# Performance work log

Measured on AMD Instinct MI355X. Metric: run time of the kernel, lower is better.

## Reference

```python
import jax, jax.numpy as jnp
import numpy as np

B, C, HGT, WID = 4096, 64, 8, 8
NUM_HEADS, HEAD_DIM = 8, 8
LN_EPS = 1e-5


def _make_chess_bias(size=8):
    idx = np.arange(size * size)
    r, c = idx // size, idx % size
    dr = np.abs(r[:, None] - r[None, :])
    dc = np.abs(c[:, None] - c[None, :])
    dist = dr + dc
    diag = dr == dc
    bias = np.where(dist == 0, 0.1, np.where(dist <= 2, 0.05, np.where(diag, 0.03, 0.0)))
    return jnp.asarray(bias, dtype=jnp.float32)


def setup_inputs() -> dict:
    key = jax.random.key(0)
    k = jax.random.split(key, 4)
    E = C
    return {
        "x": jax.random.normal(k[0], (B, C, HGT, WID), dtype=jnp.float32),
        "pos_embed": jax.random.normal(k[1], (1, C, HGT, WID), dtype=jnp.float32),
        "ln_gamma": jnp.ones((E,), dtype=jnp.float32),
        "ln_beta": jnp.zeros((E,), dtype=jnp.float32),
        "qkv_w": jax.random.normal(k[2], (3 * E, E), dtype=jnp.float32) / np.sqrt(E),
        "qkv_b": jnp.zeros((3 * E,), dtype=jnp.float32),
        "out_w": jax.random.normal(k[3], (E, E), dtype=jnp.float32) / np.sqrt(E),
        "out_b": jnp.zeros((E,), dtype=jnp.float32),
        "chess_bias": _make_chess_bias(8),
        "stage": 1,
    }


def reference(x, pos_embed, ln_gamma, ln_beta, qkv_w, qkv_b, out_w, out_b, chess_bias, stage):
    # stage is fixed (=1); params above are the stage-1 params.
    x = x + pos_embed                                   # [B, C, H, W]
    b, c, h, w = x.shape
    x_flat = x.reshape(b, c, h * w).transpose(0, 2, 1)  # [B, S, E], S = H*W
    # LayerNorm over embed dim
    mu = jnp.mean(x_flat, axis=-1, keepdims=True)
    var = jnp.var(x_flat, axis=-1, keepdims=True)
    x_norm = (x_flat - mu) * jax.lax.rsqrt(var + LN_EPS) * ln_gamma + ln_beta
    # QKV projection (torch Linear: y = x W^T + b)
    qkv = x_norm @ qkv_w.T + qkv_b                      # [B, S, 3E]
    s = h * w
    qkv = qkv.reshape(b, s, 3, NUM_HEADS, HEAD_DIM)
    q = qkv[:, :, 0].transpose(0, 2, 1, 3)              # [B, H, S, D]
    k = qkv[:, :, 1].transpose(0, 2, 1, 3)
    v = qkv[:, :, 2].transpose(0, 2, 1, 3)
    scores = jnp.einsum("bhsd,bhtd->bhst", q, k) * (HEAD_DIM ** -0.5)
    scores = scores + chess_bias[None, None, :, :]
    attn = jax.nn.softmax(scores, axis=-1)              # dropout = identity (eval)
    out = jnp.einsum("bhst,bhtd->bhsd", attn, v)        # [B, H, S, D]
    out = out.transpose(0, 2, 1, 3).reshape(b, s, c)    # [B, S, E]
    attn_out = out @ out_w.T + out_b
    x_out = x_flat + attn_out                           # residual
    return x_out.transpose(0, 2, 1).reshape(b, c, h, w)
```

## Files before the change

### kernel.cpp

```cpp
#include <hip/hip_runtime.h>
#include <stdint.h>


typedef __attribute__((ext_vector_type(8))) __bf16 bfrag;
typedef __attribute__((ext_vector_type(4))) __bf16 bf4;
typedef __attribute__((ext_vector_type(4))) float f32x4;
typedef __attribute__((ext_vector_type(4))) uint32_t u32x4;

#define MFMA16(a, b, c) __builtin_amdgcn_mfma_f32_16x16x32_bf16((a), (b), (c), 0, 0, 0)

static __device__ __forceinline__ bfrag bsplat(float v) {
  bfrag z;
#pragma unroll
  for (int i = 0; i < 8; i++) z[i] = (__bf16)v;
  return z;
}

static __device__ __forceinline__ bfrag cvt8(const float* __restrict__ p) {
  float4 a = *(const float4*)p, b = *(const float4*)(p + 4);
  bfrag r;
  r[0] = (__bf16)a.x; r[1] = (__bf16)a.y; r[2] = (__bf16)a.z; r[3] = (__bf16)a.w;
  r[4] = (__bf16)b.x; r[5] = (__bf16)b.y; r[6] = (__bf16)b.z; r[7] = (__bf16)b.w;
  return r;
}

static __device__ __forceinline__ uint32_t pack2(float a, float b) {
  unsigned short ua = __builtin_bit_cast(unsigned short, (__bf16)a);
  unsigned short ub = __builtin_bit_cast(unsigned short, (__bf16)b);
  return (uint32_t)ua | ((uint32_t)ub << 16);
}

__global__ __launch_bounds__(256, 3) void chess_attn_kernel(
    const float* __restrict__ xg,    const float* __restrict__ posg,
    const float* __restrict__ gam,   const float* __restrict__ bet,
    const float* __restrict__ qkvw,  const float* __restrict__ qkvb,
    const float* __restrict__ outw,  const float* __restrict__ outb,
    const float* __restrict__ biasg, float* __restrict__ outg) {
  __shared__ __attribute__((aligned(16))) __bf16 P1[2][64 * 136];
  __shared__ __attribute__((aligned(16))) __bf16 P2[2][64 * 72];

  const int tid = threadIdx.x, lane = tid & 63, w = tid >> 6;
  const int m = lane & 15, g = lane >> 4;
  const int b0 = blockIdx.x * 2;
  const float LN2I = 1.4426950408889634f;
  const float SCL2 = 0.35355339059327373f * LN2I;

  {
    const float4* pp = (const float4*)(posg + (size_t)lane * 64 + w * 16);
    float4 pv[4] = {pp[0], pp[1], pp[2], pp[3]};
#pragma unroll
    for (int it = 0; it < 2; it++) {
      float* XP = (float*)P1[it];
      const float4* px = (const float4*)(xg + ((size_t)(b0 + it) * 64 + lane) * 64 + w * 16);
#pragma unroll
      for (int v = 0; v < 4; v++) {
        float4 xv = px[v];
        const int s = w * 16 + v * 4;
        XP[(s + 0) * 68 + lane] = xv.x + pv[v].x;
        XP[(s + 1) * 68 + lane] = xv.y + pv[v].y;
        XP[(s + 2) * 68 + lane] = xv.z + pv[v].z;
        XP[(s + 3) * 68 + lane] = xv.w + pv[v].w;
      }
    }
  }

  {
    const int s = tid >> 2, q = tid & 3;
    const float4* pg = (const float4*)(gam + q * 16);
    const float4* pb = (const float4*)(bet + q * 16);
    float4 g0 = pg[0], g1 = pg[1], g2 = pg[2], g3 = pg[3];
    float4 b0v = pb[0], b1 = pb[1], b2 = pb[2], b3 = pb[3];
    float gr[16] = {g0.x, g0.y, g0.z, g0.w, g1.x, g1.y, g1.z, g1.w,
                    g2.x, g2.y, g2.z, g2.w, g3.x, g3.y, g3.z, g3.w};
    float br[16] = {b0v.x, b0v.y, b0v.z, b0v.w, b1.x, b1.y, b1.z, b1.w,
                    b2.x, b2.y, b2.z, b2.w, b3.x, b3.y, b3.z, b3.w};
#pragma unroll
    for (int it = 0; it < 2; it++) {
      const float* XP = (const float*)P1[it];
      const float4* pr = (const float4*)&XP[s * 68 + q * 16];
      float4 x0 = pr[0], x1 = pr[1], x2 = pr[2], x3 = pr[3];
      float xr[16] = {x0.x, x0.y, x0.z, x0.w, x1.x, x1.y, x1.z, x1.w,
                      x2.x, x2.y, x2.z, x2.w, x3.x, x3.y, x3.z, x3.w};
      float sum = 0.f, ss = 0.f;
#pragma unroll
      for (int i = 0; i < 16; i++) { sum += xr[i]; ss = fmaf(xr[i], xr[i], ss); }
      sum += __shfl_xor(sum, 1); ss += __shfl_xor(ss, 1);
      sum += __shfl_xor(sum, 2); ss += __shfl_xor(ss, 2);
      const float mu = sum * 0.015625f;
      const float rs = __builtin_amdgcn_rsqf(ss * 0.015625f - mu * mu + 1e-5f);
      bfrag o0, o1;
#pragma unroll
      for (int i = 0; i < 8; i++) o0[i] = (__bf16)((xr[i] - mu) * rs * gr[i] + br[i]);
#pragma unroll
      for (int i = 0; i < 8; i++) o1[i] = (__bf16)((xr[8 + i] - mu) * rs * gr[8 + i] + br[8 + i]);
      *(bfrag*)&P2[it][s * 72 + q * 16] = o0;
      *(bfrag*)&P2[it][s * 72 + q * 16 + 8] = o1;
    }
  }
  __syncthreads();

  bfrag XF[2][4][2];
#pragma unroll
  for (int it = 0; it < 2; it++)
#pragma unroll
    for (int st = 0; st < 4; st++) {
      XF[it][st][0] = *(const bfrag*)&P2[it][(st * 16 + m) * 72 + g * 8];
      XF[it][st][1] = *(const bfrag*)&P2[it][(st * 16 + m) * 72 + 32 + g * 8];
    }
  __syncthreads();

  {
#pragma unroll
    for (int i = 0; i < 2; i++) {
      const int nt = w + 4 * i;
      bfrag AW0 = cvt8(qkvw + (size_t)(nt * 16 + m) * 64 + g * 8);
      bfrag AW1 = cvt8(qkvw + (size_t)(nt * 16 + m) * 64 + 32 + g * 8);
      float4 qb4 = *(const float4*)(qkvb + nt * 16 + g * 4);
#pragma unroll
      for (int it = 0; it < 2; it++)
#pragma unroll
        for (int st = 0; st < 4; st++) {
          f32x4 c = {0.f, 0.f, 0.f, 0.f};
          c = MFMA16(AW0, XF[it][st][0], c);
          c = MFMA16(AW1, XF[it][st][1], c);
          bf4 pk;
          pk[0] = (__bf16)(c[0] + qb4.x); pk[1] = (__bf16)(c[1] + qb4.y);
          pk[2] = (__bf16)(c[2] + qb4.z); pk[3] = (__bf16)(c[3] + qb4.w);
          *(bf4*)&P1[it][(st * 16 + m) * 136 + nt * 16 + g * 4] = pk;
        }
    }
    {
      const int n = 128 + w * 16 + m;
      bfrag BV0 = cvt8(qkvw + (size_t)n * 64 + g * 8);
      bfrag BV1 = cvt8(qkvw + (size_t)n * 64 + 32 + g * 8);
      const float vb = qkvb[n];
#pragma unroll
      for (int it = 0; it < 2; it++)
#pragma unroll
        for (int st = 0; st < 4; st++) {
          f32x4 c = {0.f, 0.f, 0.f, 0.f};
          c = MFMA16(XF[it][st][0], BV0, c);
          c = MFMA16(XF[it][st][1], BV1, c);
          bf4 pk;
#pragma unroll
          for (int r = 0; r < 4; r++) pk[r] = (__bf16)(c[r] + vb);
          *(bf4*)&P2[it][(w * 16 + m) * 72 + st * 16 + g * 4] = pk;
        }
    }
  }
  __syncthreads();

  const bfrag ZF  = bsplat(0.f);
  const bfrag ONE = bsplat(1.f);
  const int srcA = m + 32 * (g & 1);
  const int srcB = srcA + 16;
  const bool hi = (g >= 2);
#pragma unroll 1
  for (int hl = 0; hl < 2; hl++) {
    const int h = w + hl * 4;
    bfrag KA[2][4], VA[2][2];
#pragma unroll
    for (int it = 0; it < 2; it++) {
#pragma unroll
      for (int tt = 0; tt < 4; tt++)
        KA[it][tt] = (lane < 16) ? *(const bfrag*)&P1[it][(tt * 16 + m) * 136 + 64 + h * 8] : ZF;
#pragma unroll
      for (int kf = 0; kf < 2; kf++)
        VA[it][kf] = (m < 8) ? *(const bfrag*)&P2[it][(h * 8 + m) * 72 + kf * 32 + g * 8]
                             : ((m == 8) ? ONE : ZF);
    }
#pragma unroll
    for (int st = 0; st < 4; st++) {
      float4 bv[4];
#pragma unroll
      for (int tt = 0; tt < 4; tt++)
        bv[tt] = *(const float4*)(biasg + (size_t)(st * 16 + m) * 64 + tt * 16 + g * 4);
#pragma unroll
      for (int it = 0; it < 2; it++) {
        bfrag QB = (lane < 16) ? *(const bfrag*)&P1[it][(st * 16 + m) * 136 + h * 8] : ZF;
        f32x4 sc[4];
#pragma unroll
        for (int tt = 0; tt < 4; tt++) {
          f32x4 z = {0.f, 0.f, 0.f, 0.f};
          sc[tt] = MFMA16(KA[it][tt], QB, z);
        }
        uint32_t pk[4][2];
#pragma unroll
        for (int tt = 0; tt < 4; tt++) {
          float e0 = __builtin_amdgcn_exp2f(fmaf(bv[tt].x, LN2I, sc[tt][0] * SCL2));
          float e1 = __builtin_amdgcn_exp2f(fmaf(bv[tt].y, LN2I, sc[tt][1] * SCL2));
          float e2 = __builtin_amdgcn_exp2f(fmaf(bv[tt].z, LN2I, sc[tt][2] * SCL2));
          float e3 = __builtin_amdgcn_exp2f(fmaf(bv[tt].w, LN2I, sc[tt][3] * SCL2));
          pk[tt][0] = pack2(e0, e1);
          pk[tt][1] = pack2(e2, e3);
        }
        u32x4 U0, U1;
        {
          uint32_t a0 = __shfl((int)pk[0][0], srcA), a1 = __shfl((int)pk[1][0], srcA);
          uint32_t c0 = __shfl((int)pk[0][1], srcA), c1 = __shfl((int)pk[1][1], srcA);
          uint32_t a2 = __shfl((int)pk[0][0], srcB), a3 = __shfl((int)pk[1][0], srcB);
          uint32_t c2 = __shfl((int)pk[0][1], srcB), c3 = __shfl((int)pk[1][1], srcB);
          U0[0] = hi ? a1 : a0; U0[1] = hi ? c1 : c0;
          U0[2] = hi ? a3 : a2; U0[3] = hi ? c3 : c2;
        }
        {
          uint32_t a0 = __shfl((int)pk[2][0], srcA), a1 = __shfl((int)pk[3][0], srcA);
          uint32_t c0 = __shfl((int)pk[2][1], srcA), c1 = __shfl((int)pk[3][1], srcA);
          uint32_t a2 = __shfl((int)pk[2][0], srcB), a3 = __shfl((int)pk[3][0], srcB);
          uint32_t c2 = __shfl((int)pk[2][1], srcB), c3 = __shfl((int)pk[3][1], srcB);
          U1[0] = hi ? a1 : a0; U1[1] = hi ? c1 : c0;
          U1[2] = hi ? a3 : a2; U1[3] = hi ? c3 : c2;
        }
        bfrag PB0 = __builtin_bit_cast(bfrag, U0);
        bfrag PB1 = __builtin_bit_cast(bfrag, U1);
        f32x4 oo = {0.f, 0.f, 0.f, 0.f};
        oo = MFMA16(VA[it][0], PB0, oo);
        oo = MFMA16(VA[it][1], PB1, oo);
        const float rsum = __builtin_amdgcn_rcpf(__shfl(oo[0], 32 + m));
        bf4 ov;
#pragma unroll
        for (int r = 0; r < 4; r++) ov[r] = (__bf16)(oo[r] * rsum);
        if (g < 2) *(bf4*)&P1[it][(st * 16 + m) * 136 + 64 + h * 8 + g * 4] = ov;
      }
    }
  }
  __syncthreads();

  {
    bfrag A0[2], A1[2];
#pragma unroll
    for (int it = 0; it < 2; it++) {
      A0[it] = *(const bfrag*)&P1[it][(w * 16 + m) * 136 + 64 + g * 8];
      A1[it] = *(const bfrag*)&P1[it][(w * 16 + m) * 136 + 96 + g * 8];
    }
    const int sbase = w * 16 + g * 4;
#pragma unroll
    for (int et = 0; et < 4; et++) {
      const int e = et * 16 + m;
      bfrag BW0 = cvt8(outw + (size_t)e * 64 + g * 8);
      bfrag BW1 = cvt8(outw + (size_t)e * 64 + 32 + g * 8);
      const float ob = outb[e];
      float4 pv = *(const float4*)(posg + (size_t)e * 64 + sbase);
#pragma unroll
      for (int it = 0; it < 2; it++) {
        const size_t xoff = (size_t)(b0 + it) * 4096;
        f32x4 c = {0.f, 0.f, 0.f, 0.f};
        c = MFMA16(A0[it], BW0, c);
        c = MFMA16(A1[it], BW1, c);
        float4 xv = *(const float4*)(xg + xoff + (size_t)e * 64 + sbase);
        float4 o;
        o.x = c[0] + ob + xv.x + pv.x;
        o.y = c[1] + ob + xv.y + pv.y;
        o.z = c[2] + ob + xv.z + pv.z;
        o.w = c[3] + ob + xv.w + pv.w;
        *(float4*)(outg + xoff + (size_t)e * 64 + sbase) = o;
      }
    }
  }
}

extern "C" void kernel_launch(void* const* d_in, const int* in_sizes, int n_in,
                              void* d_out, int out_size, void* d_ws, size_t ws_size,
                              hipStream_t stream) {
  const float* xg   = (const float*)d_in[0];
  const float* pos  = (const float*)d_in[1];
  const float* gam  = (const float*)d_in[2];
  const float* bet  = (const float*)d_in[3];
  const float* qkvw = (const float*)d_in[4];
  const float* qkvb = (const float*)d_in[5];
  const float* outw = (const float*)d_in[6];
  const float* outb = (const float*)d_in[7];
  const float* cb   = (const float*)d_in[8];
  float* out = (float*)d_out;
  const int B = in_sizes[0] / (64 * 64);
  hipLaunchKernelGGL(chess_attn_kernel, dim3(B / 2), dim3(256), 0, stream,
                     xg, pos, gam, bet, qkvw, qkvb, outw, outb, cb, out);
}
```

Measured before the change: 192.2 us.

## Drop P2 shared buffer, pass V via register shuffles, raise occupancy

Removes the second LDS buffer by staging the normalized input in P1 and keeping the V projection results packed in registers, then redistributing them to the attention MFMA operand layout with cross-lane shuffles. The head-to-wave mapping changes so each wave processes heads whose V columns it already holds, and one block-wide barrier is removed. Launch bounds rise to 4 blocks per SM to use the freed LDS. The cost is extra shuffles and register pressure under the tighter register budget.

```diff
diff --git a/kernel.cpp b/kernel.cpp
--- a/kernel.cpp
+++ b/kernel.cpp
@@ -30,14 +30,13 @@
   return (uint32_t)ua | ((uint32_t)ub << 16);
 }
 
-__global__ __launch_bounds__(256, 3) void chess_attn_kernel(
+__global__ __launch_bounds__(256, 4) void chess_attn_kernel(
     const float* __restrict__ xg,    const float* __restrict__ posg,
     const float* __restrict__ gam,   const float* __restrict__ bet,
     const float* __restrict__ qkvw,  const float* __restrict__ qkvb,
     const float* __restrict__ outw,  const float* __restrict__ outb,
     const float* __restrict__ biasg, float* __restrict__ outg) {
   __shared__ __attribute__((aligned(16))) __bf16 P1[2][64 * 136];
-  __shared__ __attribute__((aligned(16))) __bf16 P2[2][64 * 72];
 
   const int tid = threadIdx.x, lane = tid & 63, w = tid >> 6;
   const int m = lane & 15, g = lane >> 4;
@@ -93,8 +92,9 @@
       for (int i = 0; i < 8; i++) o0[i] = (__bf16)((xr[i] - mu) * rs * gr[i] + br[i]);
 #pragma unroll
       for (int i = 0; i < 8; i++) o1[i] = (__bf16)((xr[8 + i] - mu) * rs * gr[8 + i] + br[8 + i]);
-      *(bfrag*)&P2[it][s * 72 + q * 16] = o0;
-      *(bfrag*)&P2[it][s * 72 + q * 16 + 8] = o1;
+      __builtin_amdgcn_sched_barrier(0);
+      *(bfrag*)&P1[it][s * 136 + q * 16] = o0;
+      *(bfrag*)&P1[it][s * 136 + q * 16 + 8] = o1;
     }
   }
   __syncthreads();
@@ -104,11 +104,12 @@
   for (int it = 0; it < 2; it++)
 #pragma unroll
     for (int st = 0; st < 4; st++) {
-      XF[it][st][0] = *(const bfrag*)&P2[it][(st * 16 + m) * 72 + g * 8];
-      XF[it][st][1] = *(const bfrag*)&P2[it][(st * 16 + m) * 72 + 32 + g * 8];
+      XF[it][st][0] = *(const bfrag*)&P1[it][(st * 16 + m) * 136 + g * 8];
+      XF[it][st][1] = *(const bfrag*)&P1[it][(st * 16 + m) * 136 + 32 + g * 8];
     }
   __syncthreads();
 
+  uint32_t pk2v[2][4][2];
   {
 #pragma unroll
     for (int i = 0; i < 2; i++) {
@@ -141,33 +142,46 @@
           f32x4 c = {0.f, 0.f, 0.f, 0.f};
           c = MFMA16(XF[it][st][0], BV0, c);
           c = MFMA16(XF[it][st][1], BV1, c);
-          bf4 pk;
-#pragma unroll
-          for (int r = 0; r < 4; r++) pk[r] = (__bf16)(c[r] + vb);
-          *(bf4*)&P2[it][(w * 16 + m) * 72 + st * 16 + g * 4] = pk;
-        }
-    }
-  }
-  __syncthreads();
-
-  const bfrag ZF  = bsplat(0.f);
-  const bfrag ONE = bsplat(1.f);
+          pk2v[it][st][0] = pack2(c[0] + vb, c[1] + vb);
+          pk2v[it][st][1] = pack2(c[2] + vb, c[3] + vb);
+        }
+    }
+  }
+
+  const bfrag ZF = bsplat(0.f);
   const int srcA = m + 32 * (g & 1);
   const int srcB = srcA + 16;
   const bool hi = (g >= 2);
 #pragma unroll 1
   for (int hl = 0; hl < 2; hl++) {
-    const int h = w + hl * 4;
-    bfrag KA[2][4], VA[2][2];
+    const int h = 2 * w + hl;
+    bfrag KA[2][4];
+    u32x4 VAU[2][2];
+    const int vsrcA = ((g & 1) << 5) + 8 * hl + m;
+    const int vsrcB = vsrcA + 16;
 #pragma unroll
     for (int it = 0; it < 2; it++) {
 #pragma unroll
       for (int tt = 0; tt < 4; tt++)
         KA[it][tt] = (lane < 16) ? *(const bfrag*)&P1[it][(tt * 16 + m) * 136 + 64 + h * 8] : ZF;
 #pragma unroll
-      for (int kf = 0; kf < 2; kf++)
-        VA[it][kf] = (m < 8) ? *(const bfrag*)&P2[it][(h * 8 + m) * 72 + kf * 32 + g * 8]
-                             : ((m == 8) ? ONE : ZF);
+      for (int kf = 0; kf < 2; kf++) {
+        uint32_t a0 = (uint32_t)__shfl((int)pk2v[it][2 * kf][0], vsrcA);
+        uint32_t c0 = (uint32_t)__shfl((int)pk2v[it][2 * kf + 1][0], vsrcA);
+        uint32_t a1 = (uint32_t)__shfl((int)pk2v[it][2 * kf][1], vsrcA);
+        uint32_t c1 = (uint32_t)__shfl((int)pk2v[it][2 * kf + 1][1], vsrcA);
+        uint32_t a2 = (uint32_t)__shfl((int)pk2v[it][2 * kf][0], vsrcB);
+        uint32_t c2 = (uint32_t)__shfl((int)pk2v[it][2 * kf + 1][0], vsrcB);
+        uint32_t a3 = (uint32_t)__shfl((int)pk2v[it][2 * kf][1], vsrcB);
+        uint32_t c3 = (uint32_t)__shfl((int)pk2v[it][2 * kf + 1][1], vsrcB);
+        const uint32_t fill = (m == 8) ? 0x3F803F80u : 0u;
+        u32x4 U;
+        U[0] = (m < 8) ? (hi ? c0 : a0) : fill;
+        U[1] = (m < 8) ? (hi ? c1 : a1) : fill;
+        U[2] = (m < 8) ? (hi ? c2 : a2) : fill;
+        U[3] = (m < 8) ? (hi ? c3 : a3) : fill;
+        VAU[it][kf] = U;
+      }
     }
 #pragma unroll
     for (int st = 0; st < 4; st++) {
@@ -213,9 +227,11 @@
         }
         bfrag PB0 = __builtin_bit_cast(bfrag, U0);
         bfrag PB1 = __builtin_bit_cast(bfrag, U1);
+        bfrag VA0 = __builtin_bit_cast(bfrag, VAU[it][0]);
+        bfrag VA1 = __builtin_bit_cast(bfrag, VAU[it][1]);
         f32x4 oo = {0.f, 0.f, 0.f, 0.f};
-        oo = MFMA16(VA[it][0], PB0, oo);
-        oo = MFMA16(VA[it][1], PB1, oo);
+        oo = MFMA16(VA0, PB0, oo);
+        oo = MFMA16(VA1, PB1, oo);
         const float rsum = __builtin_amdgcn_rcpf(__shfl(oo[0], 32 + m));
         bf4 ov;
 #pragma unroll
```

New measurement: 251.6 us. 30.8% more time.

## Fold softmax scale into Q, seed MFMA with bias, stage probabilities via LDS

Applied to the files above, without the earlier changes.

Pre-multiplies Q and its bias by the scaled log2e factor at projection time. The scaled chess bias is passed as the MFMA accumulator init, so scores come out ready for exp2 with no per-element FMA. The sixteen cross-lane shuffles that re-layout the probability matrix are replaced by a bf16 write to a per-warp scratch area in P2 and two vector reads. This trades ds_bpermute traffic and select logic for plain LDS stores and loads, and relies on the reused P2 rows no longer being needed by other warps.

```diff
diff --git a/kernel.cpp b/kernel.cpp
--- a/kernel.cpp
+++ b/kernel.cpp
@@ -5,7 +5,6 @@
 typedef __attribute__((ext_vector_type(8))) __bf16 bfrag;
 typedef __attribute__((ext_vector_type(4))) __bf16 bf4;
 typedef __attribute__((ext_vector_type(4))) float f32x4;
-typedef __attribute__((ext_vector_type(4))) uint32_t u32x4;
 
 #define MFMA16(a, b, c) __builtin_amdgcn_mfma_f32_16x16x32_bf16((a), (b), (c), 0, 0, 0)
 
@@ -22,12 +21,6 @@
   r[0] = (__bf16)a.x; r[1] = (__bf16)a.y; r[2] = (__bf16)a.z; r[3] = (__bf16)a.w;
   r[4] = (__bf16)b.x; r[5] = (__bf16)b.y; r[6] = (__bf16)b.z; r[7] = (__bf16)b.w;
   return r;
-}
-
-static __device__ __forceinline__ uint32_t pack2(float a, float b) {
-  unsigned short ua = __builtin_bit_cast(unsigned short, (__bf16)a);
-  unsigned short ub = __builtin_bit_cast(unsigned short, (__bf16)b);
-  return (uint32_t)ua | ((uint32_t)ub << 16);
 }
 
 __global__ __launch_bounds__(256, 3) void chess_attn_kernel(
@@ -43,7 +36,7 @@
   const int m = lane & 15, g = lane >> 4;
   const int b0 = blockIdx.x * 2;
   const float LN2I = 1.4426950408889634f;
-  const float SCL2 = 0.35355339059327373f * LN2I;
+  const float SCL2 = 0.35355339059327373f * 1.4426950408889634f;
 
   {
     const float4* pp = (const float4*)(posg + (size_t)lane * 64 + w * 16);
@@ -116,6 +109,9 @@
       bfrag AW0 = cvt8(qkvw + (size_t)(nt * 16 + m) * 64 + g * 8);
       bfrag AW1 = cvt8(qkvw + (size_t)(nt * 16 + m) * 64 + 32 + g * 8);
       float4 qb4 = *(const float4*)(qkvb + nt * 16 + g * 4);
+      const float qs = (i == 0) ? SCL2 : 1.0f;
+      const float qbx = qb4.x * qs, qby = qb4.y * qs;
+      const float qbz = qb4.z * qs, qbw = qb4.w * qs;
 #pragma unroll
       for (int it = 0; it < 2; it++)
 #pragma unroll
@@ -124,8 +120,8 @@
           c = MFMA16(AW0, XF[it][st][0], c);
           c = MFMA16(AW1, XF[it][st][1], c);
           bf4 pk;
-          pk[0] = (__bf16)(c[0] + qb4.x); pk[1] = (__bf16)(c[1] + qb4.y);
-          pk[2] = (__bf16)(c[2] + qb4.z); pk[3] = (__bf16)(c[3] + qb4.w);
+          pk[0] = (__bf16)fmaf(c[0], qs, qbx); pk[1] = (__bf16)fmaf(c[1], qs, qby);
+          pk[2] = (__bf16)fmaf(c[2], qs, qbz); pk[3] = (__bf16)fmaf(c[3], qs, qbw);
           *(bf4*)&P1[it][(st * 16 + m) * 136 + nt * 16 + g * 4] = pk;
         }
     }
@@ -152,9 +148,8 @@
 
   const bfrag ZF  = bsplat(0.f);
   const bfrag ONE = bsplat(1.f);
-  const int srcA = m + 32 * (g & 1);
-  const int srcB = srcA + 16;
-  const bool hi = (g >= 2);
+  __bf16* PS = &P2[0][0];
+  const int rowoff = (8 * w + (m & 7)) * 72 + (m >> 3) * 4608;
 #pragma unroll 1
   for (int hl = 0; hl < 2; hl++) {
     const int h = w + hl * 4;
@@ -171,48 +166,28 @@
     }
 #pragma unroll
     for (int st = 0; st < 4; st++) {
-      float4 bv[4];
-#pragma unroll
-      for (int tt = 0; tt < 4; tt++)
-        bv[tt] = *(const float4*)(biasg + (size_t)(st * 16 + m) * 64 + tt * 16 + g * 4);
+      f32x4 binit[4];
+#pragma unroll
+      for (int tt = 0; tt < 4; tt++) {
+        float4 bv = *(const float4*)(biasg + (size_t)(st * 16 + m) * 64 + tt * 16 + g * 4);
+        binit[tt][0] = bv.x * LN2I; binit[tt][1] = bv.y * LN2I;
+        binit[tt][2] = bv.z * LN2I; binit[tt][3] = bv.w * LN2I;
+      }
 #pragma unroll
       for (int it = 0; it < 2; it++) {
         bfrag QB = (lane < 16) ? *(const bfrag*)&P1[it][(st * 16 + m) * 136 + h * 8] : ZF;
-        f32x4 sc[4];
 #pragma unroll
         for (int tt = 0; tt < 4; tt++) {
-          f32x4 z = {0.f, 0.f, 0.f, 0.f};
-          sc[tt] = MFMA16(KA[it][tt], QB, z);
+          f32x4 sc = MFMA16(KA[it][tt], QB, binit[tt]);
+          bf4 pr;
+          pr[0] = (__bf16)__builtin_amdgcn_exp2f(sc[0]);
+          pr[1] = (__bf16)__builtin_amdgcn_exp2f(sc[1]);
+          pr[2] = (__bf16)__builtin_amdgcn_exp2f(sc[2]);
+          pr[3] = (__bf16)__builtin_amdgcn_exp2f(sc[3]);
+          *(bf4*)&PS[rowoff + tt * 16 + g * 4] = pr;
         }
-        uint32_t pk[4][2];
-#pragma unroll
-        for (int tt = 0; tt < 4; tt++) {
-          float e0 = __builtin_amdgcn_exp2f(fmaf(bv[tt].x, LN2I, sc[tt][0] * SCL2));
-          float e1 = __builtin_amdgcn_exp2f(fmaf(bv[tt].y, LN2I, sc[tt][1] * SCL2));
-          float e2 = __builtin_amdgcn_exp2f(fmaf(bv[tt].z, LN2I, sc[tt][2] * SCL2));
-          float e3 = __builtin_amdgcn_exp2f(fmaf(bv[tt].w, LN2I, sc[tt][3] * SCL2));
-          pk[tt][0] = pack2(e0, e1);
-          pk[tt][1] = pack2(e2, e3);
-        }
-        u32x4 U0, U1;
-        {
-          uint32_t a0 = __shfl((int)pk[0][0], srcA), a1 = __shfl((int)pk[1][0], srcA);
-          uint32_t c0 = __shfl((int)pk[0][1], srcA), c1 = __shfl((int)pk[1][1], srcA);
-          uint32_t a2 = __shfl((int)pk[0][0], srcB), a3 = __shfl((int)pk[1][0], srcB);
-          uint32_t c2 = __shfl((int)pk[0][1], srcB), c3 = __shfl((int)pk[1][1], srcB);
-          U0[0] = hi ? a1 : a0; U0[1] = hi ? c1 : c0;
-          U0[2] = hi ? a3 : a2; U0[3] = hi ? c3 : c2;
-        }
-        {
-          uint32_t a0 = __shfl((int)pk[2][0], srcA), a1 = __shfl((int)pk[3][0], srcA);
-          uint32_t c0 = __shfl((int)pk[2][1], srcA), c1 = __shfl((int)pk[3][1], srcA);
-          uint32_t a2 = __shfl((int)pk[2][0], srcB), a3 = __shfl((int)pk[3][0], srcB);
-          uint32_t c2 = __shfl((int)pk[2][1], srcB), c3 = __shfl((int)pk[3][1], srcB);
-          U1[0] = hi ? a1 : a0; U1[1] = hi ? c1 : c0;
-          U1[2] = hi ? a3 : a2; U1[3] = hi ? c3 : c2;
-        }
-        bfrag PB0 = __builtin_bit_cast(bfrag, U0);
-        bfrag PB1 = __builtin_bit_cast(bfrag, U1);
+        bfrag PB0 = *(const bfrag*)&PS[rowoff + g * 8];
+        bfrag PB1 = *(const bfrag*)&PS[rowoff + 32 + g * 8];
         f32x4 oo = {0.f, 0.f, 0.f, 0.f};
         oo = MFMA16(VA[it][0], PB0, oo);
         oo = MFMA16(VA[it][1], PB1, oo);
```

Result: no change. 190.8 us (-0.8%).
